# Optimization experiments

Measured on AMD Instinct MI355X. Metric: run time of the kernel, lower is better.

Reference implementation:

```python
import jax, jax.numpy as jnp
import numpy as np

B, S, D = 8, 1024, 768
H, DH = 8, 96          # number_of_heads, head_outdim = D // H
DFF = 4 * D            # mlp hidden
EPS = 1e-5


def _p(key, shape, scale=0.02):
    return (jax.random.normal(key, shape, dtype=jnp.float32) * scale)


def setup_inputs() -> dict:
    key = jax.random.key(0)
    ks = jax.random.split(key, 16)
    return {
        "h": jax.random.normal(ks[0], (B, S, D), dtype=jnp.float32),
        "x": jax.random.normal(ks[1], (B, S, D), dtype=jnp.float32),
        # SLN 1: scalar gamma/beta + LayerNorm affine
        "g1": jnp.ones((), jnp.float32), "be1": jnp.zeros((), jnp.float32),
        "ln1_w": jnp.ones((D,), jnp.float32), "ln1_b": jnp.zeros((D,), jnp.float32),
        # SLN 2
        "g2": jnp.ones((), jnp.float32), "be2": jnp.zeros((), jnp.float32),
        "ln2_w": jnp.ones((D,), jnp.float32), "ln2_b": jnp.zeros((D,), jnp.float32),
        # MSA projections (stored as [in, out] for x @ W)
        "Wq": _p(ks[2], (D, H * DH)), "bq": jnp.zeros((H * DH,), jnp.float32),
        "Wk": _p(ks[3], (D, H * DH)), "bk": jnp.zeros((H * DH,), jnp.float32),
        "Wv": _p(ks[4], (D, H * DH)), "bv": jnp.zeros((H * DH,), jnp.float32),
        "Wo": _p(ks[5], (H * DH, D)), "bo": jnp.zeros((D,), jnp.float32),
        # MLP: D -> 4D -> D, relu
        "W1": _p(ks[6], (D, DFF)), "b1": jnp.zeros((DFF,), jnp.float32),
        "W2": _p(ks[7], (DFF, D)), "b2": jnp.zeros((D,), jnp.float32),
    }


def _sln(h, x, gamma, beta, w, b):
    # SLN(h, x) = gamma * x * LayerNorm(h) + beta * x
    mu = jnp.mean(h, axis=-1, keepdims=True)
    var = jnp.var(h, axis=-1, keepdims=True)
    ln = (h - mu) * jax.lax.rsqrt(var + EPS) * w + b
    return gamma * x * ln + beta * x


def _l2_msa(h, Wq, bq, Wk, bk, Wv, bv, Wo, bo):
    # L2-distance multi-head self-attention (lp=2)
    def heads(W, bias):
        y = h @ W + bias                      # [B,S,H*DH]
        return y.reshape(B, S, H, DH).transpose(0, 2, 1, 3)  # [B,H,S,DH]
    q, k, v = heads(Wq, bq), heads(Wk, bk), heads(Wv, bv)
    # pairwise L2 distances via the quadratic expansion (avoids [B,H,S,S,DH])
    q2 = jnp.sum(q * q, axis=-1)              # [B,H,S]
    k2 = jnp.sum(k * k, axis=-1)              # [B,H,S]
    qk = jnp.einsum("bhsd,bhtd->bhst", q, k)  # [B,H,S,S]
    d2 = jnp.maximum(q2[..., :, None] + k2[..., None, :] - 2.0 * qk, 0.0)
    dist = jnp.sqrt(d2)                       # cdist(q, k, p=2)
    attn = jax.nn.softmax(-dist / np.sqrt(DH), axis=-1)
    out = jnp.einsum("bhst,bhtd->bhsd", attn, v)  # [B,H,S,DH]
    out = out.transpose(0, 2, 1, 3).reshape(B, S, H * DH)
    return out @ Wo + bo


def reference(h, x, g1, be1, ln1_w, ln1_b, g2, be2, ln2_w, ln2_b,
              Wq, bq, Wk, bk, Wv, bv, Wo, bo, W1, b1, W2, b2):
    h1 = _sln(h, x, g1, be1, ln1_w, ln1_b)
    htmp = _l2_msa(h1, Wq, bq, Wk, bk, Wv, bv, Wo, bo) + h   # dropout_rate=0 -> identity
    h2 = _sln(htmp, x, g2, be2, ln2_w, ln2_b)
    hf = jax.nn.relu(h2 @ W1 + b1) @ W2 + b2 + htmp
    return (x, hf)
```

## Files before the change

kernel.cpp:

```cpp
#include <hip/hip_runtime.h>
#include <math.h>

#define B_ 8
#define S_ 1024
#define D_ 768
#define H_ 8
#define DH_ 96
#define DFF_ 3072
#define NTOK (B_*S_)
#define QKVW 2304
#define EPS_ 1e-5f

typedef __attribute__((ext_vector_type(4))) float f4;
typedef __attribute__((ext_vector_type(4))) int i4;
typedef __attribute__((ext_vector_type(8))) __bf16 bf16x8;
typedef __attribute__((ext_vector_type(4))) unsigned short us4;
typedef __attribute__((ext_vector_type(8))) unsigned short us8;

static __device__ __forceinline__ unsigned short f2bf(float f) {
    unsigned int u = __builtin_bit_cast(unsigned int, f);
    u += 0x7fffu + ((u >> 16) & 1u);
    return (unsigned short)(u >> 16);
}
static __device__ __forceinline__ float bf2f(unsigned short u) {
    unsigned int x = ((unsigned int)u) << 16;
    return __builtin_bit_cast(float, x);
}

#define GLOBAL_LOAD_LDS16(g, l) \
    __builtin_amdgcn_global_load_lds((const __attribute__((address_space(1))) unsigned int*)(g), \
                                     (__attribute__((address_space(3))) unsigned int*)(l), 16, 0, 0)

__global__ __launch_bounds__(192) void sln_kernel(
    const float* __restrict__ h, const float* __restrict__ x,
    const float* __restrict__ gamma, const float* __restrict__ beta,
    const float* __restrict__ w, const float* __restrict__ bvec,
    unsigned short* __restrict__ out_bf, float* __restrict__ xcopy)
{
    int row = blockIdx.x;
    int t = threadIdx.x;
    const float4* h4 = (const float4*)(h + (size_t)row * D_);
    const float4* x4 = (const float4*)(x + (size_t)row * D_);
    float4 hv = h4[t];
    float s  = hv.x + hv.y + hv.z + hv.w;
    float ss = hv.x*hv.x + hv.y*hv.y + hv.z*hv.z + hv.w*hv.w;
    #pragma unroll
    for (int off = 32; off > 0; off >>= 1) {
        s  += __shfl_down(s, off);
        ss += __shfl_down(ss, off);
    }
    __shared__ float red[2][3];
    int wid = t >> 6;
    if ((t & 63) == 0) { red[0][wid] = s; red[1][wid] = ss; }
    __syncthreads();
    float sum   = red[0][0] + red[0][1] + red[0][2];
    float sumsq = red[1][0] + red[1][1] + red[1][2];
    float mu  = sum * (1.0f / D_);
    float var = sumsq * (1.0f / D_) - mu * mu;
    float rstd = rsqrtf(var + EPS_);
    float g = gamma[0], be = beta[0];
    float4 wv = ((const float4*)w)[t];
    float4 bv = ((const float4*)bvec)[t];
    float4 xv = x4[t];
    us4 o;
    o.x = f2bf(xv.x * (g * ((hv.x - mu) * rstd * wv.x + bv.x) + be));
    o.y = f2bf(xv.y * (g * ((hv.y - mu) * rstd * wv.y + bv.y) + be));
    o.z = f2bf(xv.z * (g * ((hv.z - mu) * rstd * wv.z + bv.z) + be));
    o.w = f2bf(xv.w * (g * ((hv.w - mu) * rstd * wv.w + bv.w) + be));
    *(us4*)(out_bf + (size_t)row * D_ + t * 4) = o;
    if (xcopy) ((float4*)(xcopy + (size_t)row * D_))[t] = xv;
}

__global__ __launch_bounds__(256) void prep_all_kernel(
    const float* __restrict__ Wq, const float* __restrict__ Wk,
    const float* __restrict__ Wv, const float* __restrict__ Wo,
    const float* __restrict__ W1, const float* __restrict__ W2,
    const float* __restrict__ bq, const float* __restrict__ bk, const float* __restrict__ bv,
    unsigned short* __restrict__ Wqkvt, unsigned short* __restrict__ Wot,
    unsigned short* __restrict__ W1t, unsigned short* __restrict__ W2t,
    float* __restrict__ bqkv)
{
    int id = blockIdx.x;
    int tx = threadIdx.x, ty = threadIdx.y;
    if (id >= 6912) {
        int i = (id - 6912) * 256 + ty * 32 + tx;
        if (i < QKVW) {
            float v = (i < 768) ? bq[i] : (i < 1536) ? -2.f * bk[i - 768] : bv[i - 1536];
            bqkv[i] = v;
        }
        return;
    }
    const float* in; unsigned short* out; int K, N, nbx, rel;
    float scl = 1.f;
    if (id < 1728)      { int m = id / 576; rel = id % 576;
                          in = (m == 0) ? Wq : (m == 1) ? Wk : Wv;
                          if (m == 1) scl = -2.f;
                          out = Wqkvt + (size_t)m * 768 * 768; K = 768; N = 768; nbx = 24; }
    else if (id < 2304) { rel = id - 1728; in = Wo; out = Wot;  K = 768;  N = 768;  nbx = 24; }
    else if (id < 4608) { rel = id - 2304; in = W1; out = W1t;  K = 768;  N = 3072; nbx = 96; }
    else                { rel = id - 4608; in = W2; out = W2t;  K = 3072; N = 768;  nbx = 24; }
    int n0 = (rel % nbx) * 32, k0 = (rel / nbx) * 32;
    __shared__ float tile[32][33];
    #pragma unroll
    for (int r = 0; r < 4; r++)
        tile[ty + r * 8][tx] = in[(size_t)(k0 + ty + r * 8) * N + n0 + tx];
    __syncthreads();
    #pragma unroll
    for (int r = 0; r < 4; r++)
        out[(size_t)(n0 + ty + r * 8) * K + k0 + tx] = f2bf(scl * tile[tx][ty + r * 8]);
}

template<int OUT_BF16, int RELU>
__global__ __launch_bounds__(256) void gemm_mfma_kernel(
    const unsigned short* __restrict__ A, const unsigned short* __restrict__ Bt,
    const float* __restrict__ bias, const float* __restrict__ resid,
    void* __restrict__ Cout, int M, int N, int K)
{
    __shared__ unsigned short Asm[2][128 * 32];
    __shared__ unsigned short Bsm[2][128 * 32];

    int t = threadIdx.x;
    int lane = t & 63, wv = t >> 6;
    int wm = wv & 1, wn = wv >> 1;
    int l16 = lane & 15, quad = lane >> 4;

    int bm = blockIdx.x * 128;
    int bn = blockIdx.y * 128;

    const unsigned short* Abase = A  + (size_t)bm * K;
    const unsigned short* Bbase = Bt + (size_t)bn * K;

    int fl0 = t, fl1 = 256 + t;
    int r0 = fl0 >> 2, lg0 = (fl0 ^ (fl0 >> 3)) & 3;
    int r1 = fl1 >> 2, lg1 = (fl1 ^ (fl1 >> 3)) & 3;

    f4 acc[4][4] = {};

    GLOBAL_LOAD_LDS16(Abase + (size_t)r0 * K + lg0 * 8, &Asm[0][fl0 * 8]);
    GLOBAL_LOAD_LDS16(Abase + (size_t)r1 * K + lg1 * 8, &Asm[0][fl1 * 8]);
    GLOBAL_LOAD_LDS16(Bbase + (size_t)r0 * K + lg0 * 8, &Bsm[0][fl0 * 8]);
    GLOBAL_LOAD_LDS16(Bbase + (size_t)r1 * K + lg1 * 8, &Bsm[0][fl1 * 8]);
    __syncthreads();

    int nk = K >> 5;
    int cur = 0;
    for (int it = 0; it < nk; ++it) {
        if (it + 1 < nk) {
            int k0 = (it + 1) << 5;
            GLOBAL_LOAD_LDS16(Abase + (size_t)r0 * K + k0 + lg0 * 8, &Asm[cur ^ 1][fl0 * 8]);
            GLOBAL_LOAD_LDS16(Abase + (size_t)r1 * K + k0 + lg1 * 8, &Asm[cur ^ 1][fl1 * 8]);
            GLOBAL_LOAD_LDS16(Bbase + (size_t)r0 * K + k0 + lg0 * 8, &Bsm[cur ^ 1][fl0 * 8]);
            GLOBAL_LOAD_LDS16(Bbase + (size_t)r1 * K + k0 + lg1 * 8, &Bsm[cur ^ 1][fl1 * 8]);
        }

        bf16x8 xf[4], wf[4];
        #pragma unroll
        for (int i = 0; i < 4; i++) {
            int m = wm * 64 + i * 16 + l16;
            int p = (quad ^ (m >> 1)) & 3;
            xf[i] = __builtin_bit_cast(bf16x8, *(const i4*)&Asm[cur][m * 32 + p * 8]);
        }
        #pragma unroll
        for (int j = 0; j < 4; j++) {
            int n = wn * 64 + j * 16 + l16;
            int p = (quad ^ (n >> 1)) & 3;
            wf[j] = __builtin_bit_cast(bf16x8, *(const i4*)&Bsm[cur][n * 32 + p * 8]);
        }
        #pragma unroll
        for (int j = 0; j < 4; j++)
            #pragma unroll
            for (int i = 0; i < 4; i++)
                acc[j][i] = __builtin_amdgcn_mfma_f32_16x16x32_bf16(wf[j], xf[i], acc[j][i], 0, 0, 0);

        __syncthreads();
        cur ^= 1;
    }

    #pragma unroll
    for (int i = 0; i < 4; i++) {
        int rowg = bm + wm * 64 + i * 16 + l16;
        #pragma unroll
        for (int j = 0; j < 4; j++) {
            int colg0 = bn + wn * 64 + j * 16 + quad * 4;
            f4 v = acc[j][i];
            f4 b4 = *(const f4*)&bias[colg0];
            v += b4;
            if (RELU) {
                #pragma unroll
                for (int r = 0; r < 4; r++) v[r] = fmaxf(v[r], 0.f);
            }
            if (resid) {
                f4 r4 = *(const f4*)&resid[(size_t)rowg * N + colg0];
                v += r4;
            }
            if (OUT_BF16) {
                us4 o;
                o.x = f2bf(v[0]); o.y = f2bf(v[1]); o.z = f2bf(v[2]); o.w = f2bf(v[3]);
                *(us4*)((unsigned short*)Cout + (size_t)rowg * N + colg0) = o;
            } else {
                *(f4*)((float*)Cout + (size_t)rowg * N + colg0) = v;
            }
        }
    }
}

template<int OUT_BF16, int RELU>
__global__ __launch_bounds__(256) void gemm_mfma_n64_kernel(
    const unsigned short* __restrict__ A, const unsigned short* __restrict__ Bt,
    const float* __restrict__ bias, const float* __restrict__ resid,
    void* __restrict__ Cout, int M, int N, int K)
{
    __shared__ unsigned short Asm[2][128 * 64];
    __shared__ unsigned short Bsm[2][64 * 64];

    int t = threadIdx.x;
    int lane = t & 63, wv = t >> 6;
    int wm = wv & 1, wn = wv >> 1;
    int l16 = lane & 15, quad = lane >> 4;

    int bm = blockIdx.x * 128;
    int bn = blockIdx.y * 64;

    const unsigned short* Abase = A  + (size_t)bm * K;
    const unsigned short* Bbase = Bt + (size_t)bn * K;

    int ar[4], alg[4], br[2], blg[2];
    #pragma unroll
    for (int i = 0; i < 4; i++) {
        int fl = t + i * 256;
        ar[i] = fl >> 3; alg[i] = (fl ^ (fl >> 3)) & 7;
    }
    #pragma unroll
    for (int i = 0; i < 2; i++) {
        int fl = t + i * 256;
        br[i] = fl >> 3; blg[i] = (fl ^ (fl >> 3)) & 7;
    }

    f4 acc[2][4] = {};

    #pragma unroll
    for (int i = 0; i < 4; i++)
        GLOBAL_LOAD_LDS16(Abase + (size_t)ar[i] * K + alg[i] * 8, &Asm[0][(t + i * 256) * 8]);
    #pragma unroll
    for (int i = 0; i < 2; i++)
        GLOBAL_LOAD_LDS16(Bbase + (size_t)br[i] * K + blg[i] * 8, &Bsm[0][(t + i * 256) * 8]);
    __syncthreads();

    int nk = K >> 6;
    int cur = 0;
    for (int it = 0; it < nk; ++it) {
        if (it + 1 < nk) {
            int k0 = (it + 1) << 6;
            #pragma unroll
            for (int i = 0; i < 4; i++)
                GLOBAL_LOAD_LDS16(Abase + (size_t)ar[i] * K + k0 + alg[i] * 8, &Asm[cur ^ 1][(t + i * 256) * 8]);
            #pragma unroll
            for (int i = 0; i < 2; i++)
                GLOBAL_LOAD_LDS16(Bbase + (size_t)br[i] * K + k0 + blg[i] * 8, &Bsm[cur ^ 1][(t + i * 256) * 8]);
        }

        #pragma unroll
        for (int kk = 0; kk < 2; kk++) {
            bf16x8 xf[4], wf[2];
            #pragma unroll
            for (int i = 0; i < 4; i++) {
                int m = wm * 64 + i * 16 + l16;
                int p = ((kk * 4 + quad) ^ (m & 7)) & 7;
                xf[i] = __builtin_bit_cast(bf16x8, *(const i4*)&Asm[cur][m * 64 + p * 8]);
            }
            #pragma unroll
            for (int j = 0; j < 2; j++) {
                int n = wn * 32 + j * 16 + l16;
                int p = ((kk * 4 + quad) ^ (n & 7)) & 7;
                wf[j] = __builtin_bit_cast(bf16x8, *(const i4*)&Bsm[cur][n * 64 + p * 8]);
            }
            #pragma unroll
            for (int j = 0; j < 2; j++)
                #pragma unroll
                for (int i = 0; i < 4; i++)
                    acc[j][i] = __builtin_amdgcn_mfma_f32_16x16x32_bf16(wf[j], xf[i], acc[j][i], 0, 0, 0);
        }

        __syncthreads();
        cur ^= 1;
    }

    #pragma unroll
    for (int i = 0; i < 4; i++) {
        int rowg = bm + wm * 64 + i * 16 + l16;
        #pragma unroll
        for (int j = 0; j < 2; j++) {
            int colg0 = bn + wn * 32 + j * 16 + quad * 4;
            f4 v = acc[j][i];
            f4 b4 = *(const f4*)&bias[colg0];
            v += b4;
            if (RELU) {
                #pragma unroll
                for (int r = 0; r < 4; r++) v[r] = fmaxf(v[r], 0.f);
            }
            if (resid) {
                f4 r4 = *(const f4*)&resid[(size_t)rowg * N + colg0];
                v += r4;
            }
            if (OUT_BF16) {
                us4 o;
                o.x = f2bf(v[0]); o.y = f2bf(v[1]); o.z = f2bf(v[2]); o.w = f2bf(v[3]);
                *(us4*)((unsigned short*)Cout + (size_t)rowg * N + colg0) = o;
            } else {
                *(f4*)((float*)Cout + (size_t)rowg * N + colg0) = v;
            }
        }
    }
}

__global__ __launch_bounds__(256) void norms_kernel(
    const unsigned short* __restrict__ qkv, float* __restrict__ q2g, float* __restrict__ k2g)
{
    int row = blockIdx.x;
    int t = threadIdx.x;
    int hh = t >> 5, l32 = t & 31;
    const unsigned short* base = qkv + (size_t)row * QKVW + hh * DH_ + l32 * 3;
    float qs = 0.f, ks = 0.f;
    #pragma unroll
    for (int e = 0; e < 3; e++) {
        float qv = bf2f(base[e]);
        float kv = bf2f(base[768 + e]);
        qs += qv * qv; ks += kv * kv;
    }
    #pragma unroll
    for (int off = 16; off > 0; off >>= 1) {
        qs += __shfl_xor(qs, off, 32);
        ks += __shfl_xor(ks, off, 32);
    }
    if (l32 == 0) {
        int b = row >> 10, s = row & 1023;
        int idx = (b * H_ + hh) * S_ + s;
        q2g[idx] = qs; k2g[idx] = ks * 0.25f;
    }
}

__global__ __launch_bounds__(256) void vtrans_kernel(
    const unsigned short* __restrict__ qkv, unsigned short* __restrict__ vt)
{
    __shared__ unsigned short Vl[64][100];
    int blk = blockIdx.x;
    int bh = blk >> 4, kt = blk & 15;
    int b = bh >> 3, hh = bh & 7;
    int t = threadIdx.x;
    int key = t >> 2, qc = t & 3;
    const unsigned short* src = qkv + ((size_t)(b * S_ + kt * 64 + key)) * QKVW + 1536 + hh * DH_;
    #pragma unroll
    for (int i = 0; i < 3; i++) {
        int chunk = qc + i * 4;
        us8 v = *(const us8*)(src + chunk * 8);
        #pragma unroll
        for (int e = 0; e < 8; e++) Vl[key][chunk * 8 + e] = v[e];
    }
    __syncthreads();
    unsigned short* dst = vt + (size_t)blk * 7168;
    #pragma unroll
    for (int r = 0; r < 3; r++) {
        int c = r * 256 + t;
        int vd = c >> 3, kc = c & 7;
        us8 o;
        #pragma unroll
        for (int j = 0; j < 8; j++) o[j] = Vl[kc * 8 + j][vd];
        *(us8*)(dst + vd * 72 + kc * 8) = o;
    }
}

__global__ __launch_bounds__(256, 2) void attn_mfma_kernel(
    const unsigned short* __restrict__ qkv,
    const unsigned short* __restrict__ vt,
    const float* __restrict__ q2g, const float* __restrict__ k2g,
    unsigned short* __restrict__ outb)
{
    __shared__ unsigned short Klds[2][6144];
    __shared__ unsigned short Vlds[2][7168];
    __shared__ unsigned short Plds[4][2][16 * 72];

    int t = threadIdx.x;
    int lane = t & 63, w = t >> 6;
    int l16 = lane & 15, quad = lane >> 4;

    int bid = blockIdx.x;
    int slot = bid >> 3;
    int bh = (bid & 7) * 8 + (slot >> 3);
    int qt = slot & 7;
    int b = bh >> 3, hh = bh & 7;

    int qrowW = qt * 128 + w * 32;

    const unsigned short* qb = qkv + ((size_t)(b * S_ + qrowW)) * QKVW + hh * DH_;
    bf16x8 qf[2][3];
    #pragma unroll
    for (int f = 0; f < 2; f++)
        #pragma unroll
        for (int d = 0; d < 3; d++)
            qf[f][d] = __builtin_bit_cast(bf16x8,
                *(const i4*)(qb + (size_t)(f * 16 + l16) * QKVW + d * 32 + quad * 8));

    float q2n[2];
    #pragma unroll
    for (int f = 0; f < 2; f++)
        q2n[f] = q2g[bh * S_ + qrowW + f * 16 + l16];

    float lsum0 = 0.f, lsum1 = 0.f;
    f4 Oacc[2][6] = {};

    const float cexp = 0.14724445f;

    const unsigned short* kgb = qkv + ((size_t)(b * S_)) * QKVW + 768 + hh * DH_;
    const unsigned short* vgb0 = vt + (size_t)(bh * 16) * 7168;
    const float* k2base = k2g + bh * S_;

    int kkey = t & 63;
    #define ATTN_STAGE(bb, itv)                                                   \
        {                                                                         \
            _Pragma("unroll")                                                     \
            for (int r = 0; r < 3; r++) {                                         \
                int c = r * 256 + t;                                              \
                int dc = c >> 6;                                                  \
                GLOBAL_LOAD_LDS16(kgb + ((size_t)((itv) * 64 + kkey)) * QKVW + dc * 8, \
                                  &Klds[bb][c * 8]);                              \
            }                                                                     \
            const unsigned short* vgb = vgb0 + (size_t)(itv) * 7168;              \
            _Pragma("unroll")                                                     \
            for (int r = 0; r < 3; r++)                                           \
                GLOBAL_LOAD_LDS16(vgb + (r * 256 + t) * 8, &Vlds[bb][(r * 256 + t) * 8]); \
            if (t < 128)                                                          \
                GLOBAL_LOAD_LDS16(vgb + (768 + t) * 8, &Vlds[bb][(768 + t) * 8]); \
        }

    ATTN_STAGE(0, 0);
    __syncthreads();

    for (int it = 0; it < 16; it++) {
        int cur = it & 1;
        if (it) __syncthreads();
        if (it + 1 < 16) ATTN_STAGE(cur ^ 1, it + 1);

        float4 k2f[4];
        #pragma unroll
        for (int kt2 = 0; kt2 < 4; kt2++)
            k2f[kt2] = *(const float4*)(k2base + it * 64 + kt2 * 16 + quad * 4);

        const unsigned short* kB = &Klds[cur][quad * 512 + l16 * 8];
        #pragma unroll
        for (int kt2 = 0; kt2 < 4; kt2++) {
            const unsigned short* kp = kB + kt2 * 128;
            bf16x8 kf0 = __builtin_bit_cast(bf16x8, *(const i4*)(kp));
            bf16x8 kf1 = __builtin_bit_cast(bf16x8, *(const i4*)(kp + 2048));
            bf16x8 kf2 = __builtin_bit_cast(bf16x8, *(const i4*)(kp + 4096));
            #pragma unroll
            for (int f = 0; f < 2; f++) {
                f4 a = {k2f[kt2].x + q2n[f], k2f[kt2].y + q2n[f],
                        k2f[kt2].z + q2n[f], k2f[kt2].w + q2n[f]};
                a = __builtin_amdgcn_mfma_f32_16x16x32_bf16(kf0, qf[f][0], a, 0, 0, 0);
                a = __builtin_amdgcn_mfma_f32_16x16x32_bf16(kf1, qf[f][1], a, 0, 0, 0);
                a = __builtin_amdgcn_mfma_f32_16x16x32_bf16(kf2, qf[f][2], a, 0, 0, 0);
                #pragma unroll
                for (int r2 = 0; r2 < 4; r2++) {
                    float d2 = fmaxf(a[r2], 0.f);
                    float p = exp2f(-__builtin_amdgcn_sqrtf(d2) * cexp);
                    if (f == 0) lsum0 += p; else lsum1 += p;
                    a[r2] = p;
                }
                unsigned int plo, phi;
                asm("v_cvt_pk_bf16_f32 %0, %1, %2" : "=v"(plo) : "v"(a[0]), "v"(a[1]));
                asm("v_cvt_pk_bf16_f32 %0, %1, %2" : "=v"(phi) : "v"(a[2]), "v"(a[3]));
                uint2 pkd; pkd.x = plo; pkd.y = phi;
                *(uint2*)&Plds[w][f][l16 * 72 + kt2 * 16 + quad * 4] = pkd;
            }
        }
        bf16x8 pa[2][2];
        #pragma unroll
        for (int f = 0; f < 2; f++) {
            pa[f][0] = __builtin_bit_cast(bf16x8, *(const i4*)&Plds[w][f][l16 * 72 + quad * 8]);
            pa[f][1] = __builtin_bit_cast(bf16x8, *(const i4*)&Plds[w][f][l16 * 72 + 32 + quad * 8]);
        }
        #pragma unroll
        for (int vtl = 0; vtl < 6; vtl++) {
            bf16x8 vf0 = __builtin_bit_cast(bf16x8, *(const i4*)&Vlds[cur][(vtl * 16 + l16) * 72 + quad * 8]);
            bf16x8 vf1 = __builtin_bit_cast(bf16x8, *(const i4*)&Vlds[cur][(vtl * 16 + l16) * 72 + 32 + quad * 8]);
            #pragma unroll
            for (int f = 0; f < 2; f++) {
                Oacc[f][vtl] = __builtin_amdgcn_mfma_f32_16x16x32_bf16(pa[f][0], vf0, Oacc[f][vtl], 0, 0, 0);
                Oacc[f][vtl] = __builtin_amdgcn_mfma_f32_16x16x32_bf16(pa[f][1], vf1, Oacc[f][vtl], 0, 0, 0);
            }
        }
    }
    #pragma unroll
    for (int f = 0; f < 2; f++) {
        float ls = (f == 0) ? lsum0 : lsum1;
        ls += __shfl_xor(ls, 16, 64);
        ls += __shfl_xor(ls, 32, 64);
        float inv_l = 1.f / ls;
        f4 iv;
        #pragma unroll
        for (int r2 = 0; r2 < 4; r2++)
            iv[r2] = __shfl(inv_l, quad * 4 + r2, 64);
        #pragma unroll
        for (int vtl = 0; vtl < 6; vtl++)
            #pragma unroll
            for (int r2 = 0; r2 < 4; r2++) {
                int row = b * S_ + qrowW + f * 16 + quad * 4 + r2;
                outb[(size_t)row * D_ + hh * DH_ + vtl * 16 + l16] = f2bf(Oacc[f][vtl][r2] * iv[r2]);
            }
    }
    #undef ATTN_STAGE
}

extern "C" void kernel_launch(void* const* d_in, const int* in_sizes, int n_in,
                              void* d_out, int out_size, void* d_ws, size_t ws_size,
                              hipStream_t stream)
{
    const float* h    = (const float*)d_in[0];
    const float* x    = (const float*)d_in[1];
    const float* g1   = (const float*)d_in[2];
    const float* be1  = (const float*)d_in[3];
    const float* ln1w = (const float*)d_in[4];
    const float* ln1b = (const float*)d_in[5];
    const float* g2   = (const float*)d_in[6];
    const float* be2  = (const float*)d_in[7];
    const float* ln2w = (const float*)d_in[8];
    const float* ln2b = (const float*)d_in[9];
    const float* Wq   = (const float*)d_in[10];
    const float* bq   = (const float*)d_in[11];
    const float* Wk   = (const float*)d_in[12];
    const float* bk   = (const float*)d_in[13];
    const float* Wv   = (const float*)d_in[14];
    const float* bv   = (const float*)d_in[15];
    const float* Wo   = (const float*)d_in[16];
    const float* bo   = (const float*)d_in[17];
    const float* W1   = (const float*)d_in[18];
    const float* b1   = (const float*)d_in[19];
    const float* W2   = (const float*)d_in[20];
    const float* b2   = (const float*)d_in[21];

    float* out = (float*)d_out;
    char* wsb = (char*)d_ws;
    const size_t ND = (size_t)NTOK * D_;

    size_t off = 0;
    unsigned short* W1t = (unsigned short*)(wsb + off); off += 4718592;
    unsigned short* W2t = (unsigned short*)(wsb + off); off += 4718592;
    float* bqkv = (float*)(wsb + off);                  off += 16384;
    float* htmp = (float*)(wsb + off);                  off += ND * 4;
    float* q2g  = (float*)(wsb + off);                  off += (size_t)B_ * H_ * S_ * 4;
    float* k2g  = (float*)(wsb + off);                  off += (size_t)B_ * H_ * S_ * 4;
    unsigned short* h2b = (unsigned short*)(wsb + off); off += ND * 2;
    size_t pool0 = off;
    unsigned short* Wqkvt = (unsigned short*)(wsb + off); off += 3538944;
    unsigned short* Wot   = (unsigned short*)(wsb + off); off += 1179648;
    unsigned short* h1b   = (unsigned short*)(wsb + off); off += ND * 2;
    unsigned short* vtg   = (unsigned short*)(wsb + off); off += (size_t)1024 * 14336;
    unsigned short* qkvb  = (unsigned short*)(wsb + off); off += (size_t)NTOK * QKVW * 2;
    unsigned short* attnb   = h1b;
    unsigned short* hiddenb = (unsigned short*)(wsb + pool0);

    prep_all_kernel<<<6921, dim3(32, 8), 0, stream>>>(
        Wq, Wk, Wv, Wo, W1, W2, bq, bk, bv, Wqkvt, Wot, W1t, W2t, bqkv);

    sln_kernel<<<NTOK, 192, 0, stream>>>(h, x, g1, be1, ln1w, ln1b, h1b, out);

    gemm_mfma_kernel<1, 0><<<dim3(NTOK/128, QKVW/128), 256, 0, stream>>>(
        h1b, Wqkvt, bqkv, nullptr, qkvb, NTOK, QKVW, D_);

    norms_kernel<<<NTOK, 256, 0, stream>>>(qkvb, q2g, k2g);
    vtrans_kernel<<<1024, 256, 0, stream>>>(qkvb, vtg);

    attn_mfma_kernel<<<512, 256, 0, stream>>>(qkvb, vtg, q2g, k2g, attnb);

    gemm_mfma_n64_kernel<0, 0><<<dim3(NTOK/128, D_/64), 256, 0, stream>>>(
        attnb, Wot, bo, h, htmp, NTOK, D_, D_);

    sln_kernel<<<NTOK, 192, 0, stream>>>(htmp, x, g2, be2, ln2w, ln2b, h2b, nullptr);

    gemm_mfma_kernel<1, 1><<<dim3(NTOK/128, DFF_/128), 256, 0, stream>>>(
        h2b, W1t, b1, nullptr, hiddenb, NTOK, DFF_, D_);
    gemm_mfma_n64_kernel<0, 0><<<dim3(NTOK/128, D_/64), 256, 0, stream>>>(
        hiddenb, W2t, b2, htmp, out + ND, NTOK, D_, DFF_);

    (void)in_sizes; (void)n_in; (void)out_size; (void)ws_size;
}
```

Baseline: 425.1 us.

## Fold softmax scale into Q/K weights, fuse norms into vtrans, add 256-row MLP GEMM

Folds the exp2 softmax scale into the prepped Wq/Wk weights and biases, which removes the per-element multiply and clamp in attention; a fabs replaces the clamp at zero. The separate norms kernel is merged into the V-transpose kernel, saving one launch and a second read of Q/K. Attention now stages k2 into LDS asynchronously and raises wave priority around the MFMA blocks. The MLP up-projection moves to a new 512-thread GEMM with 256x128 tiles to get more reuse per block. Since the squared norms are computed from scaled bf16 Q/K, rounding changes slightly.

```diff
diff --git a/kernel.cpp b/kernel.cpp
--- a/kernel.cpp
+++ b/kernel.cpp
@@ -10,6 +10,7 @@
 #define NTOK (B_*S_)
 #define QKVW 2304
 #define EPS_ 1e-5f
+#define CEXP_ 0.14724445f
 
 typedef __attribute__((ext_vector_type(4))) float f4;
 typedef __attribute__((ext_vector_type(4))) int i4;
@@ -85,7 +86,8 @@
     if (id >= 6912) {
         int i = (id - 6912) * 256 + ty * 32 + tx;
         if (i < QKVW) {
-            float v = (i < 768) ? bq[i] : (i < 1536) ? -2.f * bk[i - 768] : bv[i - 1536];
+            float v = (i < 768) ? CEXP_ * bq[i]
+                    : (i < 1536) ? -2.f * CEXP_ * bk[i - 768] : bv[i - 1536];
             bqkv[i] = v;
         }
         return;
@@ -94,7 +96,8 @@
     float scl = 1.f;
     if (id < 1728)      { int m = id / 576; rel = id % 576;
                           in = (m == 0) ? Wq : (m == 1) ? Wk : Wv;
-                          if (m == 1) scl = -2.f;
+                          if (m == 0) scl = CEXP_;
+                          if (m == 1) scl = -2.f * CEXP_;
                           out = Wqkvt + (size_t)m * 768 * 768; K = 768; N = 768; nbx = 24; }
     else if (id < 2304) { rel = id - 1728; in = Wo; out = Wot;  K = 768;  N = 768;  nbx = 24; }
     else if (id < 4608) { rel = id - 2304; in = W1; out = W1t;  K = 768;  N = 3072; nbx = 96; }
@@ -205,6 +208,99 @@
 }
 
 template<int OUT_BF16, int RELU>
+__global__ __launch_bounds__(512, 4) void gemm_mfma_m256_kernel(
+    const unsigned short* __restrict__ A, const unsigned short* __restrict__ Bt,
+    const float* __restrict__ bias, const float* __restrict__ resid,
+    void* __restrict__ Cout, int M, int N, int K)
+{
+    __shared__ unsigned short Asm[2][256 * 32];
+    __shared__ unsigned short Bsm[2][128 * 32];
+
+    int t = threadIdx.x;
+    int lane = t & 63, wv = t >> 6;
+    int wm = wv & 3, wn = wv >> 2;
+    int l16 = lane & 15, quad = lane >> 4;
+
+    int bm = blockIdx.x * 256;
+    int bn = blockIdx.y * 128;
+
+    const unsigned short* Abase = A  + (size_t)bm * K;
+    const unsigned short* Bbase = Bt + (size_t)bn * K;
+
+    int fa0 = t, fa1 = t + 512;
+    int ra0 = fa0 >> 2, la0 = (fa0 ^ (fa0 >> 3)) & 3;
+    int ra1 = fa1 >> 2, la1 = (fa1 ^ (fa1 >> 3)) & 3;
+    int rb0 = t >> 2,   lb0 = (t ^ (t >> 3)) & 3;
+
+    f4 acc[4][4] = {};
+
+    GLOBAL_LOAD_LDS16(Abase + (size_t)ra0 * K + la0 * 8, &Asm[0][fa0 * 8]);
+    GLOBAL_LOAD_LDS16(Abase + (size_t)ra1 * K + la1 * 8, &Asm[0][fa1 * 8]);
+    GLOBAL_LOAD_LDS16(Bbase + (size_t)rb0 * K + lb0 * 8, &Bsm[0][t * 8]);
+    __syncthreads();
+
+    int nk = K >> 5;
+    int cur = 0;
+    for (int it = 0; it < nk; ++it) {
+        if (it + 1 < nk) {
+            int k0 = (it + 1) << 5;
+            GLOBAL_LOAD_LDS16(Abase + (size_t)ra0 * K + k0 + la0 * 8, &Asm[cur ^ 1][fa0 * 8]);
+            GLOBAL_LOAD_LDS16(Abase + (size_t)ra1 * K + k0 + la1 * 8, &Asm[cur ^ 1][fa1 * 8]);
+            GLOBAL_LOAD_LDS16(Bbase + (size_t)rb0 * K + k0 + lb0 * 8, &Bsm[cur ^ 1][t * 8]);
+        }
+
+        bf16x8 xf[4], wf[4];
+        #pragma unroll
+        for (int i = 0; i < 4; i++) {
+            int m = wm * 64 + i * 16 + l16;
+            int p = (quad ^ (m >> 1)) & 3;
+            xf[i] = __builtin_bit_cast(bf16x8, *(const i4*)&Asm[cur][m * 32 + p * 8]);
+        }
+        #pragma unroll
+        for (int j = 0; j < 4; j++) {
+            int n = wn * 64 + j * 16 + l16;
+            int p = (quad ^ (n >> 1)) & 3;
+            wf[j] = __builtin_bit_cast(bf16x8, *(const i4*)&Bsm[cur][n * 32 + p * 8]);
+        }
+        #pragma unroll
+        for (int j = 0; j < 4; j++)
+            #pragma unroll
+            for (int i = 0; i < 4; i++)
+                acc[j][i] = __builtin_amdgcn_mfma_f32_16x16x32_bf16(wf[j], xf[i], acc[j][i], 0, 0, 0);
+
+        __syncthreads();
+        cur ^= 1;
+    }
+
+    #pragma unroll
+    for (int i = 0; i < 4; i++) {
+        int rowg = bm + wm * 64 + i * 16 + l16;
+        #pragma unroll
+        for (int j = 0; j < 4; j++) {
+            int colg0 = bn + wn * 64 + j * 16 + quad * 4;
+            f4 v = acc[j][i];
+            f4 b4 = *(const f4*)&bias[colg0];
+            v += b4;
+            if (RELU) {
+                #pragma unroll
+                for (int r = 0; r < 4; r++) v[r] = fmaxf(v[r], 0.f);
+            }
+            if (resid) {
+                f4 r4 = *(const f4*)&resid[(size_t)rowg * N + colg0];
+                v += r4;
+            }
+            if (OUT_BF16) {
+                us4 o;
+                o.x = f2bf(v[0]); o.y = f2bf(v[1]); o.z = f2bf(v[2]); o.w = f2bf(v[3]);
+                *(us4*)((unsigned short*)Cout + (size_t)rowg * N + colg0) = o;
+            } else {
+                *(f4*)((float*)Cout + (size_t)rowg * N + colg0) = v;
+            }
+        }
+    }
+}
+
+template<int OUT_BF16, int RELU>
 __global__ __launch_bounds__(256) void gemm_mfma_n64_kernel(
     const unsigned short* __restrict__ A, const unsigned short* __restrict__ Bt,
     const float* __restrict__ bias, const float* __restrict__ resid,
@@ -313,34 +409,9 @@
     }
 }
 
-__global__ __launch_bounds__(256) void norms_kernel(
-    const unsigned short* __restrict__ qkv, float* __restrict__ q2g, float* __restrict__ k2g)
-{
-    int row = blockIdx.x;
-    int t = threadIdx.x;
-    int hh = t >> 5, l32 = t & 31;
-    const unsigned short* base = qkv + (size_t)row * QKVW + hh * DH_ + l32 * 3;
-    float qs = 0.f, ks = 0.f;
-    #pragma unroll
-    for (int e = 0; e < 3; e++) {
-        float qv = bf2f(base[e]);
-        float kv = bf2f(base[768 + e]);
-        qs += qv * qv; ks += kv * kv;
-    }
-    #pragma unroll
-    for (int off = 16; off > 0; off >>= 1) {
-        qs += __shfl_xor(qs, off, 32);
-        ks += __shfl_xor(ks, off, 32);
-    }
-    if (l32 == 0) {
-        int b = row >> 10, s = row & 1023;
-        int idx = (b * H_ + hh) * S_ + s;
-        q2g[idx] = qs; k2g[idx] = ks * 0.25f;
-    }
-}
-
-__global__ __launch_bounds__(256) void vtrans_kernel(
-    const unsigned short* __restrict__ qkv, unsigned short* __restrict__ vt)
+__global__ __launch_bounds__(256) void vtrans_norms_kernel(
+    const unsigned short* __restrict__ qkv, unsigned short* __restrict__ vt,
+    float* __restrict__ q2g, float* __restrict__ k2g)
 {
     __shared__ unsigned short Vl[64][100];
     int blk = blockIdx.x;
@@ -348,7 +419,25 @@
     int b = bh >> 3, hh = bh & 7;
     int t = threadIdx.x;
     int key = t >> 2, qc = t & 3;
-    const unsigned short* src = qkv + ((size_t)(b * S_ + kt * 64 + key)) * QKVW + 1536 + hh * DH_;
+    const unsigned short* tok = qkv + ((size_t)(b * S_ + kt * 64 + key)) * QKVW + hh * DH_;
+    float qs = 0.f, ks = 0.f;
+    #pragma unroll
+    for (int i = 0; i < 3; i++) {
+        us8 qv = *(const us8*)(tok + (qc * 3 + i) * 8);
+        us8 kv = *(const us8*)(tok + 768 + (qc * 3 + i) * 8);
+        #pragma unroll
+        for (int e = 0; e < 8; e++) {
+            float qf = bf2f(qv[e]), kf = bf2f(kv[e]);
+            qs += qf * qf; ks += kf * kf;
+        }
+    }
+    qs += __shfl_xor(qs, 1, 4); qs += __shfl_xor(qs, 2, 4);
+    ks += __shfl_xor(ks, 1, 4); ks += __shfl_xor(ks, 2, 4);
+    if (qc == 0) {
+        int idx = (b * H_ + hh) * S_ + kt * 64 + key;
+        q2g[idx] = qs; k2g[idx] = ks * 0.25f;
+    }
+    const unsigned short* src = tok + 1536;
     #pragma unroll
     for (int i = 0; i < 3; i++) {
         int chunk = qc + i * 4;
@@ -377,6 +466,7 @@
 {
     __shared__ unsigned short Klds[2][6144];
     __shared__ unsigned short Vlds[2][7168];
+    __shared__ float k2lds[2][64];
     __shared__ unsigned short Plds[4][2][16 * 72];
 
     int t = threadIdx.x;
@@ -407,8 +497,6 @@
 
     float lsum0 = 0.f, lsum1 = 0.f;
     f4 Oacc[2][6] = {};
-
-    const float cexp = 0.14724445f;
 
     const unsigned short* kgb = qkv + ((size_t)(b * S_)) * QKVW + 768 + hh * DH_;
     const unsigned short* vgb0 = vt + (size_t)(bh * 16) * 7168;
@@ -430,6 +518,8 @@
                 GLOBAL_LOAD_LDS16(vgb + (r * 256 + t) * 8, &Vlds[bb][(r * 256 + t) * 8]); \
             if (t < 128)                                                          \
                 GLOBAL_LOAD_LDS16(vgb + (768 + t) * 8, &Vlds[bb][(768 + t) * 8]); \
+            if (t < 16)                                                           \
+                GLOBAL_LOAD_LDS16(k2base + (itv) * 64 + t * 4, &k2lds[bb][t * 4]); \
         }
 
     ATTN_STAGE(0, 0);
@@ -439,11 +529,6 @@
         int cur = it & 1;
         if (it) __syncthreads();
         if (it + 1 < 16) ATTN_STAGE(cur ^ 1, it + 1);
-
-        float4 k2f[4];
-        #pragma unroll
-        for (int kt2 = 0; kt2 < 4; kt2++)
-            k2f[kt2] = *(const float4*)(k2base + it * 64 + kt2 * 16 + quad * 4);
 
         const unsigned short* kB = &Klds[cur][quad * 512 + l16 * 8];
         #pragma unroll
@@ -452,17 +537,18 @@
             bf16x8 kf0 = __builtin_bit_cast(bf16x8, *(const i4*)(kp));
             bf16x8 kf1 = __builtin_bit_cast(bf16x8, *(const i4*)(kp + 2048));
             bf16x8 kf2 = __builtin_bit_cast(bf16x8, *(const i4*)(kp + 4096));
+            f4 kk = *(const f4*)&k2lds[cur][kt2 * 16 + quad * 4];
             #pragma unroll
             for (int f = 0; f < 2; f++) {
-                f4 a = {k2f[kt2].x + q2n[f], k2f[kt2].y + q2n[f],
-                        k2f[kt2].z + q2n[f], k2f[kt2].w + q2n[f]};
+                f4 a = {kk[0] + q2n[f], kk[1] + q2n[f], kk[2] + q2n[f], kk[3] + q2n[f]};
+                __builtin_amdgcn_s_setprio(1);
                 a = __builtin_amdgcn_mfma_f32_16x16x32_bf16(kf0, qf[f][0], a, 0, 0, 0);
                 a = __builtin_amdgcn_mfma_f32_16x16x32_bf16(kf1, qf[f][1], a, 0, 0, 0);
                 a = __builtin_amdgcn_mfma_f32_16x16x32_bf16(kf2, qf[f][2], a, 0, 0, 0);
+                __builtin_amdgcn_s_setprio(0);
                 #pragma unroll
                 for (int r2 = 0; r2 < 4; r2++) {
-                    float d2 = fmaxf(a[r2], 0.f);
-                    float p = exp2f(-__builtin_amdgcn_sqrtf(d2) * cexp);
+                    float p = exp2f(-__builtin_amdgcn_sqrtf(__builtin_fabsf(a[r2])));
                     if (f == 0) lsum0 += p; else lsum1 += p;
                     a[r2] = p;
                 }
@@ -479,6 +565,7 @@
             pa[f][0] = __builtin_bit_cast(bf16x8, *(const i4*)&Plds[w][f][l16 * 72 + quad * 8]);
             pa[f][1] = __builtin_bit_cast(bf16x8, *(const i4*)&Plds[w][f][l16 * 72 + 32 + quad * 8]);
         }
+        __builtin_amdgcn_s_setprio(1);
         #pragma unroll
         for (int vtl = 0; vtl < 6; vtl++) {
             bf16x8 vf0 = __builtin_bit_cast(bf16x8, *(const i4*)&Vlds[cur][(vtl * 16 + l16) * 72 + quad * 8]);
@@ -489,6 +576,7 @@
                 Oacc[f][vtl] = __builtin_amdgcn_mfma_f32_16x16x32_bf16(pa[f][1], vf1, Oacc[f][vtl], 0, 0, 0);
             }
         }
+        __builtin_amdgcn_s_setprio(0);
     }
     #pragma unroll
     for (int f = 0; f < 2; f++) {
@@ -567,8 +655,7 @@
     gemm_mfma_kernel<1, 0><<<dim3(NTOK/128, QKVW/128), 256, 0, stream>>>(
         h1b, Wqkvt, bqkv, nullptr, qkvb, NTOK, QKVW, D_);
 
-    norms_kernel<<<NTOK, 256, 0, stream>>>(qkvb, q2g, k2g);
-    vtrans_kernel<<<1024, 256, 0, stream>>>(qkvb, vtg);
+    vtrans_norms_kernel<<<1024, 256, 0, stream>>>(qkvb, vtg, q2g, k2g);
 
     attn_mfma_kernel<<<512, 256, 0, stream>>>(qkvb, vtg, q2g, k2g, attnb);
 
@@ -577,7 +664,7 @@
 
     sln_kernel<<<NTOK, 192, 0, stream>>>(htmp, x, g2, be2, ln2w, ln2b, h2b, nullptr);
 
-    gemm_mfma_kernel<1, 1><<<dim3(NTOK/128, DFF_/128), 256, 0, stream>>>(
+    gemm_mfma_m256_kernel<1, 1><<<dim3(NTOK/256, DFF_/128), 512, 0, stream>>>(
         h2b, W1t, b1, nullptr, hiddenb, NTOK, DFF_, D_);
     gemm_mfma_n64_kernel<0, 0><<<dim3(NTOK/128, D_/64), 256, 0, stream>>>(
         hiddenb, W2t, b2, htmp, out + ND, NTOK, D_, DFF_);
```

Result: faster. 405.6 us (-4.6%).
